# Performance work log

Measured on AMD Instinct MI355X. Metric: run time of the kernel, lower is better.

## Reference

```python
import jax, jax.numpy as jnp
import numpy as np

# Static graph structure: gene nodes first, GO-term nodes last (mask is sorted).
N_GENE, N_GOID = 40000, 10000
N = N_GENE + N_GOID
E = 800000
INPUT_DIM, H1, H2, OUT_DIM, GOID_DIM = 1280, 256, 128, 64, 4096


def setup_inputs() -> dict:
    key = jax.random.key(0)
    ks = jax.random.split(key, 16)
    s = 0.02
    return {
        "x": jax.random.normal(ks[0], (N, GOID_DIM), jnp.float32),
        "edge_index": jax.random.randint(ks[1], (2, E), 0, N),
        "mask": jnp.concatenate([jnp.ones(N_GENE, bool), jnp.zeros(N_GOID, bool)]),
        # goid_dnn: Linear(4096,1024) -> ReLU -> Linear(1024,INPUT_DIM) -> ReLU
        "Wd1": jax.random.normal(ks[2], (GOID_DIM, 1024), jnp.float32) * s,
        "bd1": jnp.zeros((1024,), jnp.float32),
        "Wd2": jax.random.normal(ks[3], (1024, INPUT_DIM), jnp.float32) * s,
        "bd2": jnp.zeros((INPUT_DIM,), jnp.float32),
        # GCNConv layers
        "W1": jax.random.normal(ks[4], (INPUT_DIM, H1), jnp.float32) * s,
        "b1": jnp.zeros((H1,), jnp.float32),
        "W2": jax.random.normal(ks[5], (H1, H2), jnp.float32) * s,
        "b2": jnp.zeros((H2,), jnp.float32),
        # goid projections
        "Wp1": jax.random.normal(ks[6], (INPUT_DIM, H1), jnp.float32) * s,
        "bp1": jnp.zeros((H1,), jnp.float32),
        "Wp2": jax.random.normal(ks[7], (H1, H2), jnp.float32) * s,
        "bp2": jnp.zeros((H2,), jnp.float32),
        # final fc
        "Wf": jax.random.normal(ks[8], (H2, OUT_DIM), jnp.float32) * s,
        "bf": jnp.zeros((OUT_DIM,), jnp.float32),
    }


def gcn_conv(x, W, b, src, dst):
    """PyG GCNConv: xW, then sym-normalized (A + I) aggregation, then bias."""
    # degree over targets with self-loops already appended to (src, dst)
    deg = jax.ops.segment_sum(jnp.ones_like(dst, x.dtype), dst, num_segments=N)
    dinv = jnp.where(deg > 0, jax.lax.rsqrt(deg), 0.0)
    norm = dinv[src] * dinv[dst]                       # [E+N]
    xw = x @ W                                          # [N, F_out]
    msg = xw[src] * norm[:, None]                       # gather-scale, [E+N, F_out]
    return jax.ops.segment_sum(msg, dst, num_segments=N) + b


def reference(x, edge_index, mask, Wd1, bd1, Wd2, bd2, W1, b1, W2, b2,
              Wp1, bp1, Wp2, bp2, Wf, bf):
    del mask  # structurally: first N_GENE rows are genes, rest are GO terms
    loop = jnp.arange(N, dtype=edge_index.dtype)
    src = jnp.concatenate([edge_index[0], loop])
    dst = jnp.concatenate([edge_index[1], loop])

    gene_x = x[:N_GENE, :INPUT_DIM]
    goid_x = x[N_GENE:]
    # goid_dnn runs under torch.no_grad() -> stop_gradient
    goid_t = jax.lax.stop_gradient(
        jax.nn.relu(jax.nn.relu(goid_x @ Wd1 + bd1) @ Wd2 + bd2))

    x_t = jnp.concatenate([gene_x, goid_t], axis=0)      # [N, INPUT_DIM]
    h1 = jax.nn.relu(gcn_conv(x_t, W1, b1, src, dst))    # dropout disabled (eval)
    p1 = goid_t @ Wp1 + bp1                              # goid_proj1
    h1 = h1.at[N_GENE:].set(p1)                          # masked scatter assign
    h2 = jax.nn.relu(gcn_conv(h1, W2, b2, src, dst))
    h2 = h2.at[N_GENE:].set(p1 @ Wp2 + bp2)              # goid_proj2(goid_proj1(...))
    return h2 @ Wf + bf                                  # [N, OUT_DIM]
```

## Files before the change

kernel.cpp:

```cpp
#include <hip/hip_runtime.h>

constexpr int kNGene = 40000;
constexpr int kNGoid = 10000;
constexpr int kN     = 50000;
constexpr int kE     = 800000;
constexpr int kInDim = 1280;
constexpr int kH1    = 256;
constexpr int kH2    = 128;
constexpr int kOut   = 64;
constexpr int kGDim  = 4096;
constexpr int kD1    = 1024;

typedef short bf16x8 __attribute__((ext_vector_type(8)));
typedef float f32x4  __attribute__((ext_vector_type(4)));

static __device__ __forceinline__ short f2bf(float f) {
  union { float f; unsigned u; } v; v.f = f;
  unsigned r = v.u + 0x7FFF + ((v.u >> 16) & 1);
  return (short)(r >> 16);
}
static __device__ __forceinline__ float bf2f(short s) {
  union { unsigned u; float f; } v;
  v.u = ((unsigned)(unsigned short)s) << 16;
  return v.f;
}
static __device__ __forceinline__ void gld16(const void* g, void* l) {
  __builtin_amdgcn_global_load_lds(
      (const __attribute__((address_space(1))) void*)g,
      (__attribute__((address_space(3))) void*)l, 16, 0, 0);
}

__global__ __launch_bounds__(256)
void k_cvt_rows(const float* __restrict__ src, int lda, short* __restrict__ dst,
                int rows, int cols) {
  int chunks_per_row = cols >> 3;
  long long total = (long long)rows * chunks_per_row;
  long long stride = (long long)gridDim.x * blockDim.x;
  for (long long i = blockIdx.x * (long long)blockDim.x + threadIdx.x; i < total; i += stride) {
    int r = (int)(i / chunks_per_row);
    int c = (int)(i - (long long)r * chunks_per_row) << 3;
    const float* sp = src + (size_t)r * lda + c;
    float4 v0 = *reinterpret_cast<const float4*>(sp);
    float4 v1 = *reinterpret_cast<const float4*>(sp + 4);
    bf16x8 t;
    t[0]=f2bf(v0.x); t[1]=f2bf(v0.y); t[2]=f2bf(v0.z); t[3]=f2bf(v0.w);
    t[4]=f2bf(v1.x); t[5]=f2bf(v1.y); t[6]=f2bf(v1.z); t[7]=f2bf(v1.w);
    *reinterpret_cast<bf16x8*>(dst + (size_t)r * cols + c) = t;
  }
}

__global__ void k_init(float* deg, int* gcount) {
  int i = blockIdx.x * blockDim.x + threadIdx.x;
  if (i < kN) deg[i] = 1.0f;
  if (i == 0) *gcount = 0;
}
__global__ void k_deg_hist(const int* __restrict__ ei, float* __restrict__ deg) {
  int e = blockIdx.x * blockDim.x + threadIdx.x;
  if (e < kE) atomicAdd(&deg[ei[kE + e]], 1.0f);
}
__global__ void k_rowassign(const float* __restrict__ deg, int* __restrict__ rowstart,
                            int* __restrict__ cursor, int* __restrict__ gcount) {
  int i = blockIdx.x * blockDim.x + threadIdx.x;
  int lane = threadIdx.x & 63;
  int c = (i < kNGene) ? ((int)deg[i] - 1) : 0;
  int incl = c;
#pragma unroll
  for (int off = 1; off < 64; off <<= 1) {
    int t = __shfl_up(incl, off, 64);
    if (lane >= off) incl += t;
  }
  int total = __shfl(incl, 63, 64);
  int base = 0;
  if (lane == 63) base = atomicAdd(gcount, total);
  base = __shfl(base, 63, 64);
  if (i < kNGene) {
    int s = base + incl - c;
    rowstart[i] = s;
    cursor[i] = s;
  }
}
__global__ void k_fill(const int* __restrict__ ei, const float* __restrict__ deg,
                       int* __restrict__ cursor, int2* __restrict__ edges) {
  int e = blockIdx.x * blockDim.x + threadIdx.x;
  if (e >= kE) return;
  int dst = ei[kE + e];
  if (dst >= kNGene) return;
  int src = ei[e];
  int pos = atomicAdd(&cursor[dst], 1);
  float nrm = rsqrtf(deg[src] * deg[dst]);
  edges[pos] = make_int2(src, __float_as_int(nrm));
}

template <int F, int OBF>
__global__ __launch_bounds__(256)
void k_gather_bf(const short* __restrict__ xw, const float* __restrict__ deg,
                 const int* __restrict__ rowstart, const int2* __restrict__ edges,
                 const float* __restrict__ bias, void* __restrict__ hv) {
  constexpr int VEC = F / 64;
  int row = (blockIdx.x * blockDim.x + threadIdx.x) >> 6;
  int lane = threadIdx.x & 63;
  if (row >= kNGene) return;
  float dg = deg[row];
  float inv = 1.0f / dg;
  float acc[VEC];
  {
    const short* xr = xw + (size_t)row * F + lane * VEC;
    if constexpr (VEC == 4) {
      short4 s = *reinterpret_cast<const short4*>(xr);
      acc[0] = bf2f(s.x) * inv; acc[1] = bf2f(s.y) * inv;
      acc[2] = bf2f(s.z) * inv; acc[3] = bf2f(s.w) * inv;
    } else {
      short2 s = *reinterpret_cast<const short2*>(xr);
      acc[0] = bf2f(s.x) * inv; acc[1] = bf2f(s.y) * inv;
    }
  }
  const int2* ep = edges + rowstart[row];
  int n = (int)dg - 1;
  int e = 0;
  for (; e + 1 < n; e += 2) {
    int2 p0 = ep[e], p1 = ep[e + 1];
    float n0 = __int_as_float(p0.y), n1 = __int_as_float(p1.y);
    const short* x0 = xw + (size_t)p0.x * F + lane * VEC;
    const short* x1 = xw + (size_t)p1.x * F + lane * VEC;
    if constexpr (VEC == 4) {
      short4 s0 = *reinterpret_cast<const short4*>(x0);
      short4 s1 = *reinterpret_cast<const short4*>(x1);
      acc[0] += bf2f(s0.x) * n0; acc[1] += bf2f(s0.y) * n0;
      acc[2] += bf2f(s0.z) * n0; acc[3] += bf2f(s0.w) * n0;
      acc[0] += bf2f(s1.x) * n1; acc[1] += bf2f(s1.y) * n1;
      acc[2] += bf2f(s1.z) * n1; acc[3] += bf2f(s1.w) * n1;
    } else {
      short2 s0 = *reinterpret_cast<const short2*>(x0);
      short2 s1 = *reinterpret_cast<const short2*>(x1);
      acc[0] += bf2f(s0.x) * n0; acc[1] += bf2f(s0.y) * n0;
      acc[0] += bf2f(s1.x) * n1; acc[1] += bf2f(s1.y) * n1;
    }
  }
  if (e < n) {
    int2 p0 = ep[e];
    float n0 = __int_as_float(p0.y);
    const short* x0 = xw + (size_t)p0.x * F + lane * VEC;
    if constexpr (VEC == 4) {
      short4 s0 = *reinterpret_cast<const short4*>(x0);
      acc[0] += bf2f(s0.x) * n0; acc[1] += bf2f(s0.y) * n0;
      acc[2] += bf2f(s0.z) * n0; acc[3] += bf2f(s0.w) * n0;
    } else {
      short2 s0 = *reinterpret_cast<const short2*>(x0);
      acc[0] += bf2f(s0.x) * n0; acc[1] += bf2f(s0.y) * n0;
    }
  }
#pragma unroll
  for (int v = 0; v < VEC; ++v) acc[v] = fmaxf(acc[v] + bias[lane * VEC + v], 0.f);
  if constexpr (OBF) {
    short* hp = (short*)hv + (size_t)row * F + lane * VEC;
    if constexpr (VEC == 4) {
      short4 o; o.x = f2bf(acc[0]); o.y = f2bf(acc[1]); o.z = f2bf(acc[2]); o.w = f2bf(acc[3]);
      *reinterpret_cast<short4*>(hp) = o;
    } else {
      short2 o; o.x = f2bf(acc[0]); o.y = f2bf(acc[1]);
      *reinterpret_cast<short2*>(hp) = o;
    }
  } else {
    float* hp = (float*)hv + (size_t)row * F + lane * VEC;
    if constexpr (VEC == 4) {
      float4 o; o.x = acc[0]; o.y = acc[1]; o.z = acc[2]; o.w = acc[3];
      *reinterpret_cast<float4*>(hp) = o;
    } else {
      float2 o; o.x = acc[0]; o.y = acc[1];
      *reinterpret_cast<float2*>(hp) = o;
    }
  }
}

__global__ __launch_bounds__(256)
void k_wtrans(const float* __restrict__ W, short* __restrict__ Wt, int K, int N) {
  __shared__ float t[32][33];
  int tx = threadIdx.x & 31, ty = threadIdx.x >> 5;
  int n0 = blockIdx.x * 32, k0 = blockIdx.y * 32;
#pragma unroll
  for (int p = 0; p < 4; ++p)
    t[ty + 8 * p][tx] = W[(size_t)(k0 + ty + 8 * p) * N + n0 + tx];
  __syncthreads();
#pragma unroll
  for (int p = 0; p < 4; ++p)
    Wt[(size_t)(n0 + ty + 8 * p) * K + k0 + tx] = f2bf(t[tx][ty + 8 * p]);
}

template <int RELU, int OBF>
__global__ __launch_bounds__(256)
void k_gemm_bf16a(const short* __restrict__ A, int lda,
                  const short* __restrict__ Bt,
                  const float* __restrict__ bias,
                  void* __restrict__ Cv, int ldc,
                  short* __restrict__ C2,
                  int M, int K)
{
  __shared__ __align__(16) short As[2][128 * 32];
  __shared__ __align__(16) short Bs[2][128 * 32];
  const int tid  = threadIdx.x;
  const int lane = tid & 63;
  const int wid  = tid >> 6;
  const int wr = wid >> 1, wc = wid & 1;
  const int row0 = blockIdx.y * 128;
  const int col0 = blockIdx.x * 128;
  const int l15 = lane & 15, l4 = lane >> 4;
  const int srow = lane >> 2, schunk = lane & 3;

  f32x4 acc[4][4] = {};

  auto stage = [&](int buf, int k0) {
#pragma unroll
    for (int q = 0; q < 2; ++q) {
      int seg = wid * 2 + q;
      int r = seg * 16 + srow;
      int grow = row0 + r;
      if (grow >= M) grow = M - 1;
      gld16(A + (size_t)grow * lda + k0 + schunk * 8, &As[buf][seg * 512]);
      int gcol = col0 + r;
      gld16(Bt + (size_t)gcol * K + k0 + schunk * 8, &Bs[buf][seg * 512]);
    }
  };

  stage(0, 0);
  __syncthreads();
  int cur = 0;
  for (int k0 = 0; k0 < K; k0 += 32) {
    if (k0 + 32 < K) stage(cur ^ 1, k0 + 32);
    bf16x8 af[4], bfr[4];
#pragma unroll
    for (int m = 0; m < 4; ++m)
      af[m] = *reinterpret_cast<bf16x8*>(&As[cur][(wr * 64 + m * 16 + l15) * 32 + l4 * 8]);
#pragma unroll
    for (int n = 0; n < 4; ++n)
      bfr[n] = *reinterpret_cast<bf16x8*>(&Bs[cur][(wc * 64 + n * 16 + l15) * 32 + l4 * 8]);
#pragma unroll
    for (int m = 0; m < 4; ++m)
#pragma unroll
      for (int n = 0; n < 4; ++n)
        acc[m][n] = __builtin_amdgcn_mfma_f32_16x16x32_bf16(af[m], bfr[n], acc[m][n], 0, 0, 0);
    __syncthreads();
    cur ^= 1;
  }

#pragma unroll
  for (int n = 0; n < 4; ++n) {
    int col = col0 + wc * 64 + n * 16 + l15;
    float bv = bias ? bias[col] : 0.f;
#pragma unroll
    for (int m = 0; m < 4; ++m) {
      int rb = row0 + wr * 64 + m * 16 + l4 * 4;
#pragma unroll
      for (int e = 0; e < 4; ++e) {
        int r = rb + e;
        if (r < M) {
          float v = acc[m][n][e] + bv;
          if (RELU) v = fmaxf(v, 0.f);
          size_t idx = (size_t)r * ldc + col;
          if constexpr (OBF) ((short*)Cv)[idx] = f2bf(v);
          else {
            ((float*)Cv)[idx] = v;
            if (C2) C2[idx] = f2bf(v);
          }
        }
      }
    }
  }
}

__global__ __launch_bounds__(256)
void k_gemm_combo(const short* __restrict__ A, int lda,
                  const short* __restrict__ Bt,
                  const float* __restrict__ bp1,
                  short* __restrict__ X1, float* __restrict__ P1,
                  short* __restrict__ H1, int M, int K)
{
  __shared__ __align__(16) short As[2][128 * 32];
  __shared__ __align__(16) short Bs[2][128 * 32];
  const int tid  = threadIdx.x;
  const int lane = tid & 63;
  const int wid  = tid >> 6;
  const int wr = wid >> 1, wc = wid & 1;
  const int row0 = blockIdx.y * 128;
  const int col0 = blockIdx.x * 128;
  const int l15 = lane & 15, l4 = lane >> 4;
  const int srow = lane >> 2, schunk = lane & 3;

  f32x4 acc[4][4] = {};

  auto stage = [&](int buf, int k0) {
#pragma unroll
    for (int q = 0; q < 2; ++q) {
      int seg = wid * 2 + q;
      int r = seg * 16 + srow;
      int grow = row0 + r;
      if (grow >= M) grow = M - 1;
      gld16(A + (size_t)grow * lda + k0 + schunk * 8, &As[buf][seg * 512]);
      int gcol = col0 + r;
      gld16(Bt + (size_t)gcol * K + k0 + schunk * 8, &Bs[buf][seg * 512]);
    }
  };

  stage(0, 0);
  __syncthreads();
  int cur = 0;
  for (int k0 = 0; k0 < K; k0 += 32) {
    if (k0 + 32 < K) stage(cur ^ 1, k0 + 32);
    bf16x8 af[4], bfr[4];
#pragma unroll
    for (int m = 0; m < 4; ++m)
      af[m] = *reinterpret_cast<bf16x8*>(&As[cur][(wr * 64 + m * 16 + l15) * 32 + l4 * 8]);
#pragma unroll
    for (int n = 0; n < 4; ++n)
      bfr[n] = *reinterpret_cast<bf16x8*>(&Bs[cur][(wc * 64 + n * 16 + l15) * 32 + l4 * 8]);
#pragma unroll
    for (int m = 0; m < 4; ++m)
#pragma unroll
      for (int n = 0; n < 4; ++n)
        acc[m][n] = __builtin_amdgcn_mfma_f32_16x16x32_bf16(af[m], bfr[n], acc[m][n], 0, 0, 0);
    __syncthreads();
    cur ^= 1;
  }

  const int is_p1 = (col0 >= 256);
#pragma unroll
  for (int n = 0; n < 4; ++n) {
    int col = col0 + wc * 64 + n * 16 + l15;
    int cl = col - (is_p1 ? 256 : 0);
    float bv = is_p1 ? bp1[cl] : 0.f;
#pragma unroll
    for (int m = 0; m < 4; ++m) {
      int rb = row0 + wr * 64 + m * 16 + l4 * 4;
#pragma unroll
      for (int e = 0; e < 4; ++e) {
        int r = rb + e;
        if (r < M) {
          float v = acc[m][n][e] + bv;
          size_t idx = (size_t)r * 256 + cl;
          if (is_p1) { P1[idx] = v; H1[idx] = f2bf(v); }
          else       { X1[idx] = f2bf(v); }
        }
      }
    }
  }
}

__global__ __launch_bounds__(512)
void k_gemm_gene(const float* __restrict__ A, int lda,
                 const short* __restrict__ Bt,
                 short* __restrict__ C,
                 int M, int K)
{
  __shared__ short As[128 * 40];
  __shared__ __align__(16) short Bs[256 * 32];
  const int tid  = threadIdx.x;
  const int lane = tid & 63;
  const int wid  = tid >> 6;
  const int wr = wid >> 2;
  const int wc = wid & 3;
  const int row0 = blockIdx.x * 128;
  const int l15 = lane & 15, l4 = lane >> 4;

  f32x4 acc[4][4] = {};
  const int sr = tid >> 2;
  const int sc = tid & 3;
  const int srow = lane >> 2, schunk = lane & 3;

  for (int k0 = 0; k0 < K; k0 += 32) {
#pragma unroll
    for (int q = 0; q < 2; ++q) {
      int seg = wid * 2 + q;
      int gcol = seg * 16 + srow;
      gld16(Bt + (size_t)gcol * K + k0 + schunk * 8, &Bs[seg * 512]);
    }
    {
      int grow = row0 + sr;
      float4 v0 = make_float4(0.f,0.f,0.f,0.f), v1 = v0;
      if (grow < M) {
        const float* ap = A + (size_t)grow * lda + k0 + sc * 8;
        v0 = *reinterpret_cast<const float4*>(ap);
        v1 = *reinterpret_cast<const float4*>(ap + 4);
      }
      bf16x8 t;
      t[0]=f2bf(v0.x); t[1]=f2bf(v0.y); t[2]=f2bf(v0.z); t[3]=f2bf(v0.w);
      t[4]=f2bf(v1.x); t[5]=f2bf(v1.y); t[6]=f2bf(v1.z); t[7]=f2bf(v1.w);
      *reinterpret_cast<bf16x8*>(&As[sr * 40 + sc * 8]) = t;
    }
    __syncthreads();

    bf16x8 af[4], bfr[4];
#pragma unroll
    for (int m = 0; m < 4; ++m)
      af[m] = *reinterpret_cast<bf16x8*>(&As[(wr * 64 + m * 16 + l15) * 40 + l4 * 8]);
#pragma unroll
    for (int n = 0; n < 4; ++n)
      bfr[n] = *reinterpret_cast<bf16x8*>(&Bs[(wc * 64 + n * 16 + l15) * 32 + l4 * 8]);
#pragma unroll
    for (int m = 0; m < 4; ++m)
#pragma unroll
      for (int n = 0; n < 4; ++n)
        acc[m][n] = __builtin_amdgcn_mfma_f32_16x16x32_bf16(af[m], bfr[n], acc[m][n], 0, 0, 0);
    __syncthreads();
  }

#pragma unroll
  for (int n = 0; n < 4; ++n) {
    int col = wc * 64 + n * 16 + l15;
#pragma unroll
    for (int m = 0; m < 4; ++m) {
      int rb = row0 + wr * 64 + m * 16 + l4 * 4;
#pragma unroll
      for (int e = 0; e < 4; ++e) {
        int r = rb + e;
        if (r < M) C[(size_t)r * 256 + col] = f2bf(acc[m][n][e]);
      }
    }
  }
}

__global__ __launch_bounds__(256)
void k_gemm_f32(const float* __restrict__ A, int lda,
                const float* __restrict__ B, int ldb,
                const float* __restrict__ bias,
                float* __restrict__ C, int ldc,
                int M, int Ncol, int K, int do_relu)
{
  __shared__ float As[16][65];
  __shared__ float Bs[16][68];
  const int tid = threadIdx.x;
  const int tx = tid & 15, ty = tid >> 4;
  const int row0 = blockIdx.y * 64;
  const int col0 = blockIdx.x * 64;
  float acc[4][4] = {};
  for (int k0 = 0; k0 < K; k0 += 16) {
    {
      int r = tid >> 2;
      int c = (tid & 3) << 2;
      int grow = row0 + r;
      float4 v = make_float4(0.f, 0.f, 0.f, 0.f);
      if (grow < M)
        v = *reinterpret_cast<const float4*>(A + (size_t)grow * lda + k0 + c);
      As[c + 0][r] = v.x; As[c + 1][r] = v.y; As[c + 2][r] = v.z; As[c + 3][r] = v.w;
    }
    {
      int r = tid >> 4;
      int c = (tid & 15) << 2;
      int gcol = col0 + c;
      float4 v = make_float4(0.f, 0.f, 0.f, 0.f);
      if (gcol < Ncol)
        v = *reinterpret_cast<const float4*>(B + (size_t)(k0 + r) * ldb + gcol);
      *reinterpret_cast<float4*>(&Bs[r][c]) = v;
    }
    __syncthreads();
#pragma unroll
    for (int k = 0; k < 16; ++k) {
      float a[4], b[4];
#pragma unroll
      for (int i = 0; i < 4; ++i) a[i] = As[k][ty + 16 * i];
#pragma unroll
      for (int j = 0; j < 4; ++j) b[j] = Bs[k][tx + 16 * j];
#pragma unroll
      for (int i = 0; i < 4; ++i)
#pragma unroll
        for (int j = 0; j < 4; ++j)
          acc[i][j] = fmaf(a[i], b[j], acc[i][j]);
    }
    __syncthreads();
  }
#pragma unroll
  for (int i = 0; i < 4; ++i) {
    int r = row0 + ty + 16 * i;
    if (r >= M) continue;
#pragma unroll
    for (int j = 0; j < 4; ++j) {
      int ccol = col0 + tx + 16 * j;
      if (ccol >= Ncol) continue;
      float v = acc[i][j];
      if (bias) v += bias[ccol];
      if (do_relu) v = fmaxf(v, 0.f);
      C[(size_t)r * ldc + ccol] = v;
    }
  }
}

extern "C" void kernel_launch(void* const* d_in, const int* in_sizes, int n_in,
                              void* d_out, int out_size, void* d_ws, size_t ws_size,
                              hipStream_t stream) {
  const float* x   = (const float*)d_in[0];
  const int*   ei  = (const int*)d_in[1];
  const float* Wd1 = (const float*)d_in[3];
  const float* bd1 = (const float*)d_in[4];
  const float* Wd2 = (const float*)d_in[5];
  const float* bd2 = (const float*)d_in[6];
  const float* W1  = (const float*)d_in[7];
  const float* b1  = (const float*)d_in[8];
  const float* W2  = (const float*)d_in[9];
  const float* b2  = (const float*)d_in[10];
  const float* Wp1 = (const float*)d_in[11];
  const float* bp1 = (const float*)d_in[12];
  const float* Wp2 = (const float*)d_in[13];
  const float* bp2 = (const float*)d_in[14];
  const float* Wf  = (const float*)d_in[15];
  const float* bf_ = (const float*)d_in[16];
  float* out = (float*)d_out;
  float* ws  = (float*)d_ws;

  short* goidx_bf = (short*)(ws + 0);
  short* goidt_bf = (short*)(ws + 20480000);
  short* h1tmp_bf = (short*)(ws + 26880000);
  short* Wd1t = (short*)(ws + 32000000);
  short* Wd2t = (short*)(ws + 34097152);
  short* W1t  = (short*)(ws + 34752512);
  short* Wp1t = (short*)(ws + 34916352);
  short* W2t  = (short*)(ws + 35080192);
  short* xw1_bf = (short*)(ws + 35100000);
  short* h1bf   = (short*)(ws + 41500000);
  float* p1     = ws + 47900000;
  short* xw2_bf = (short*)(ws + 50460000);
  float* h2     = ws + 53660000;
  float* deg    = ws + 60060000;
  int*   rowstart = (int*)(ws + 60150016);
  int*   cursor   = (int*)(ws + 60190016);
  int2*  edges    = (int2*)(ws + 60230016);
  int*   gcount   = (int*)(ws + 61830016);

  const float* gene_x = x;
  const float* goid_x = x + (size_t)kNGene * kGDim;

  auto gb = [](int M, int Ncol) { return dim3((unsigned)(Ncol / 128), (unsigned)((M + 127) / 128)); };
  auto gf = [](int M, int Ncol) { return dim3((unsigned)((Ncol + 63) / 64), (unsigned)((M + 63) / 64)); };

  k_cvt_rows<<<2048, 256, 0, stream>>>(goid_x, kGDim, goidx_bf, kNGoid, kGDim);
  k_wtrans<<<dim3(kD1 / 32, kGDim / 32), 256, 0, stream>>>(Wd1, Wd1t, kGDim, kD1);
  k_wtrans<<<dim3(kInDim / 32, kD1 / 32), 256, 0, stream>>>(Wd2, Wd2t, kD1, kInDim);
  k_wtrans<<<dim3(kH1 / 32, kInDim / 32), 256, 0, stream>>>(W1, W1t, kInDim, kH1);
  k_wtrans<<<dim3(kH1 / 32, kInDim / 32), 256, 0, stream>>>(Wp1, Wp1t, kInDim, kH1);
  k_wtrans<<<dim3(kH2 / 32, kH1 / 32), 256, 0, stream>>>(W2, W2t, kH1, kH2);

  k_init<<<(kN + 255) / 256, 256, 0, stream>>>(deg, gcount);
  k_deg_hist<<<(kE + 255) / 256, 256, 0, stream>>>(ei, deg);
  k_rowassign<<<(kNGene + 255) / 256, 256, 0, stream>>>(deg, rowstart, cursor, gcount);
  k_fill<<<(kE + 255) / 256, 256, 0, stream>>>(ei, deg, cursor, edges);

  k_gemm_bf16a<1,1><<<gb(kNGoid, kD1), 256, 0, stream>>>(goidx_bf, kGDim, Wd1t, bd1,
                                                         h1tmp_bf, kD1, nullptr, kNGoid, kGDim);
  k_gemm_bf16a<1,1><<<gb(kNGoid, kInDim), 256, 0, stream>>>(h1tmp_bf, kD1, Wd2t, bd2,
                                                            goidt_bf, kInDim, nullptr, kNGoid, kD1);

  k_gemm_gene<<<dim3((kNGene + 127) / 128), 512, 0, stream>>>(gene_x, kGDim, W1t,
                                                              xw1_bf, kNGene, kInDim);

  k_gemm_combo<<<dim3(4, (kNGoid + 127) / 128), 256, 0, stream>>>(
      goidt_bf, kInDim, W1t , bp1,
      xw1_bf + (size_t)kNGene * kH1, p1, h1bf + (size_t)kNGene * kH1,
      kNGoid, kInDim);

  k_gather_bf<kH1,1><<<(kNGene * 64 + 255) / 256, 256, 0, stream>>>(
      xw1_bf, deg, rowstart, edges, b1, h1bf);

  k_gemm_bf16a<0,1><<<gb(kN, kH2), 256, 0, stream>>>(h1bf, kH1, W2t, nullptr,
                                                     xw2_bf, kH2, nullptr, kN, kH1);

  k_gather_bf<kH2,0><<<(kNGene * 64 + 255) / 256, 256, 0, stream>>>(
      xw2_bf, deg, rowstart, edges, b2, h2);
  k_gemm_f32<<<gf(kNGoid, kH2), 256, 0, stream>>>(p1, kH1, Wp2, kH2, bp2,
                                                  h2 + (size_t)kNGene * kH2, kH2,
                                                  kNGoid, kH2, kH1, 0);

  k_gemm_f32<<<gf(kN, kOut), 256, 0, stream>>>(h2, kH2, Wf, kOut, bf_, out, kOut,
                                               kN, kOut, kH2, 0);
}
```

Measured before the change: 684.1 us.

## Widen GEMM tiles, double-buffer gene GEMM, merge weight transposes, bf16 proj2

The five weight-transpose launches become one kernel that also transposes Wp2. The goid DNN GEMMs and the combo GEMM move to 128x256 tiles with 512 threads, and the DNN GEMMs get an XCD-aware block swizzle. The gene GEMM gains double-buffered LDS staging so loads overlap MFMA. The fp32 P1 buffer is dropped, and proj2 now runs as a bf16 MFMA GEMM on the bf16 copy of p1, which adds rounding error in exchange for less memory traffic and fewer launches.

```diff
diff --git a/kernel.cpp b/kernel.cpp
--- a/kernel.cpp
+++ b/kernel.cpp
@@ -173,10 +173,24 @@
 }
 
 __global__ __launch_bounds__(256)
-void k_wtrans(const float* __restrict__ W, short* __restrict__ Wt, int K, int N) {
+void k_wtrans_all(const float* __restrict__ Wd1, short* __restrict__ Wd1t,
+                  const float* __restrict__ Wd2, short* __restrict__ Wd2t,
+                  const float* __restrict__ W1,  short* __restrict__ W1t,
+                  const float* __restrict__ Wp1, short* __restrict__ Wp1t,
+                  const float* __restrict__ W2,  short* __restrict__ W2t,
+                  const float* __restrict__ Wp2, short* __restrict__ Wp2t) {
   __shared__ float t[32][33];
+  int b = blockIdx.x;
+  const float* W; short* Wt; int K, N, bi;
+  if (b < 4096)      { W = Wd1; Wt = Wd1t; K = 4096; N = 1024; bi = b; }
+  else if (b < 5376) { W = Wd2; Wt = Wd2t; K = 1024; N = 1280; bi = b - 4096; }
+  else if (b < 5696) { W = W1;  Wt = W1t;  K = 1280; N = 256;  bi = b - 5376; }
+  else if (b < 6016) { W = Wp1; Wt = Wp1t; K = 1280; N = 256;  bi = b - 5696; }
+  else if (b < 6048) { W = W2;  Wt = W2t;  K = 256;  N = 128;  bi = b - 6016; }
+  else               { W = Wp2; Wt = Wp2t; K = 256;  N = 128;  bi = b - 6048; }
+  int nbx = N >> 5;
+  int n0 = (bi % nbx) * 32, k0 = (bi / nbx) * 32;
   int tx = threadIdx.x & 31, ty = threadIdx.x >> 5;
-  int n0 = blockIdx.x * 32, k0 = blockIdx.y * 32;
 #pragma unroll
   for (int p = 0; p < 4; ++p)
     t[ty + 8 * p][tx] = W[(size_t)(k0 + ty + 8 * p) * N + n0 + tx];
@@ -192,7 +206,6 @@
                   const short* __restrict__ Bt,
                   const float* __restrict__ bias,
                   void* __restrict__ Cv, int ldc,
-                  short* __restrict__ C2,
                   int M, int K)
 {
   __shared__ __align__(16) short As[2][128 * 32];
@@ -257,31 +270,33 @@
           if (RELU) v = fmaxf(v, 0.f);
           size_t idx = (size_t)r * ldc + col;
           if constexpr (OBF) ((short*)Cv)[idx] = f2bf(v);
-          else {
-            ((float*)Cv)[idx] = v;
-            if (C2) C2[idx] = f2bf(v);
-          }
+          else               ((float*)Cv)[idx] = v;
         }
       }
     }
   }
 }
 
-__global__ __launch_bounds__(256)
-void k_gemm_combo(const short* __restrict__ A, int lda,
-                  const short* __restrict__ Bt,
-                  const float* __restrict__ bp1,
-                  short* __restrict__ X1, float* __restrict__ P1,
-                  short* __restrict__ H1, int M, int K)
+template <int RELU, int OBF>
+__global__ __launch_bounds__(512)
+void k_gemm_wide(const short* __restrict__ A, int lda,
+                 const short* __restrict__ Bt,
+                 const float* __restrict__ bias,
+                 void* __restrict__ Cv, int ldc,
+                 int M, int K)
 {
   __shared__ __align__(16) short As[2][128 * 32];
-  __shared__ __align__(16) short Bs[2][128 * 32];
+  __shared__ __align__(16) short Bs[2][256 * 32];
   const int tid  = threadIdx.x;
   const int lane = tid & 63;
   const int wid  = tid >> 6;
-  const int wr = wid >> 1, wc = wid & 1;
-  const int row0 = blockIdx.y * 128;
-  const int col0 = blockIdx.x * 128;
+  const int wr = wid >> 2, wc = wid & 3;
+  int nwg = gridDim.x * gridDim.y;
+  int b0 = blockIdx.y * gridDim.x + blockIdx.x;
+  int qq = nwg >> 3, rr = nwg & 7, xcd = b0 & 7, j = b0 >> 3;
+  int swz = ((xcd < rr) ? xcd * (qq + 1) : rr * (qq + 1) + (xcd - rr) * qq) + j;
+  const int row0 = (swz / gridDim.x) * 128;
+  const int col0 = (swz % gridDim.x) * 256;
   const int l15 = lane & 15, l4 = lane >> 4;
   const int srow = lane >> 2, schunk = lane & 3;
 
@@ -289,14 +304,16 @@
 
   auto stage = [&](int buf, int k0) {
 #pragma unroll
-    for (int q = 0; q < 2; ++q) {
-      int seg = wid * 2 + q;
-      int r = seg * 16 + srow;
-      int grow = row0 + r;
-      if (grow >= M) grow = M - 1;
-      gld16(A + (size_t)grow * lda + k0 + schunk * 8, &As[buf][seg * 512]);
-      int gcol = col0 + r;
-      gld16(Bt + (size_t)gcol * K + k0 + schunk * 8, &Bs[buf][seg * 512]);
+    for (int q = 0; q < 3; ++q) {
+      int s = wid * 3 + q;
+      if (s < 8) {
+        int grow = row0 + s * 16 + srow;
+        if (grow >= M) grow = M - 1;
+        gld16(A + (size_t)grow * lda + k0 + schunk * 8, &As[buf][s * 512]);
+      } else {
+        int gcol = col0 + (s - 8) * 16 + srow;
+        gld16(Bt + (size_t)gcol * K + k0 + schunk * 8, &Bs[buf][(s - 8) * 512]);
+      }
     }
   };
 
@@ -321,12 +338,10 @@
     cur ^= 1;
   }
 
-  const int is_p1 = (col0 >= 256);
 #pragma unroll
   for (int n = 0; n < 4; ++n) {
     int col = col0 + wc * 64 + n * 16 + l15;
-    int cl = col - (is_p1 ? 256 : 0);
-    float bv = is_p1 ? bp1[cl] : 0.f;
+    float bv = bias ? bias[col] : 0.f;
 #pragma unroll
     for (int m = 0; m < 4; ++m) {
       int rb = row0 + wr * 64 + m * 16 + l4 * 4;
@@ -335,10 +350,85 @@
         int r = rb + e;
         if (r < M) {
           float v = acc[m][n][e] + bv;
-          size_t idx = (size_t)r * 256 + cl;
-          if (is_p1) { P1[idx] = v; H1[idx] = f2bf(v); }
-          else       { X1[idx] = f2bf(v); }
+          if (RELU) v = fmaxf(v, 0.f);
+          size_t idx = (size_t)r * ldc + col;
+          if constexpr (OBF) ((short*)Cv)[idx] = f2bf(v);
+          else               ((float*)Cv)[idx] = v;
         }
+      }
+    }
+  }
+}
+
+__global__ __launch_bounds__(512)
+void k_combo_wide(const short* __restrict__ A, int lda,
+                  const short* __restrict__ Bt,
+                  const float* __restrict__ bp1,
+                  short* __restrict__ X1, short* __restrict__ H1,
+                  int M, int K)
+{
+  __shared__ __align__(16) short As[2][128 * 32];
+  __shared__ __align__(16) short Bs[2][256 * 32];
+  const int tid  = threadIdx.x;
+  const int lane = tid & 63;
+  const int wid  = tid >> 6;
+  const int wr = wid >> 2, wc = wid & 3;
+  const int row0 = blockIdx.y * 128;
+  const int col0 = blockIdx.x * 256;
+  const int l15 = lane & 15, l4 = lane >> 4;
+  const int srow = lane >> 2, schunk = lane & 3;
+
+  f32x4 acc[4][4] = {};
+
+  auto stage = [&](int buf, int k0) {
+#pragma unroll
+    for (int q = 0; q < 3; ++q) {
+      int s = wid * 3 + q;
+      if (s < 8) {
+        int grow = row0 + s * 16 + srow;
+        if (grow >= M) grow = M - 1;
+        gld16(A + (size_t)grow * lda + k0 + schunk * 8, &As[buf][s * 512]);
+      } else {
+        int gcol = col0 + (s - 8) * 16 + srow;
+        gld16(Bt + (size_t)gcol * K + k0 + schunk * 8, &Bs[buf][(s - 8) * 512]);
+      }
+    }
+  };
+
+  stage(0, 0);
+  __syncthreads();
+  int cur = 0;
+  for (int k0 = 0; k0 < K; k0 += 32) {
+    if (k0 + 32 < K) stage(cur ^ 1, k0 + 32);
+    bf16x8 af[4], bfr[4];
+#pragma unroll
+    for (int m = 0; m < 4; ++m)
+      af[m] = *reinterpret_cast<bf16x8*>(&As[cur][(wr * 64 + m * 16 + l15) * 32 + l4 * 8]);
+#pragma unroll
+    for (int n = 0; n < 4; ++n)
+      bfr[n] = *reinterpret_cast<bf16x8*>(&Bs[cur][(wc * 64 + n * 16 + l15) * 32 + l4 * 8]);
+#pragma unroll
+    for (int m = 0; m < 4; ++m)
+#pragma unroll
+      for (int n = 0; n < 4; ++n)
+        acc[m][n] = __builtin_amdgcn_mfma_f32_16x16x32_bf16(af[m], bfr[n], acc[m][n], 0, 0, 0);
+    __syncthreads();
+    cur ^= 1;
+  }
+
+  const int is_p1 = (col0 >= 256);
+  short* dstp = is_p1 ? H1 : X1;
+#pragma unroll
+  for (int n = 0; n < 4; ++n) {
+    int cl = wc * 64 + n * 16 + l15;
+    float bv = is_p1 ? bp1[cl] : 0.f;
+#pragma unroll
+    for (int m = 0; m < 4; ++m) {
+      int rb = row0 + wr * 64 + m * 16 + l4 * 4;
+#pragma unroll
+      for (int e = 0; e < 4; ++e) {
+        int r = rb + e;
+        if (r < M) dstp[(size_t)r * 256 + cl] = f2bf(acc[m][n][e] + bv);
       }
     }
   }
@@ -350,56 +440,60 @@
                  short* __restrict__ C,
                  int M, int K)
 {
-  __shared__ short As[128 * 40];
-  __shared__ __align__(16) short Bs[256 * 32];
+  __shared__ short As[2][128 * 40];
+  __shared__ __align__(16) short Bs[2][256 * 32];
   const int tid  = threadIdx.x;
   const int lane = tid & 63;
   const int wid  = tid >> 6;
-  const int wr = wid >> 2;
-  const int wc = wid & 3;
+  const int wr = wid >> 2, wc = wid & 3;
   const int row0 = blockIdx.x * 128;
   const int l15 = lane & 15, l4 = lane >> 4;
+  const int sr = tid >> 2, sc = tid & 3;
+  const int srow = lane >> 2, schunk = lane & 3;
 
   f32x4 acc[4][4] = {};
-  const int sr = tid >> 2;
-  const int sc = tid & 3;
-  const int srow = lane >> 2, schunk = lane & 3;
-
-  for (int k0 = 0; k0 < K; k0 += 32) {
+
+  auto stageB = [&](int buf, int k0) {
 #pragma unroll
     for (int q = 0; q < 2; ++q) {
       int seg = wid * 2 + q;
       int gcol = seg * 16 + srow;
-      gld16(Bt + (size_t)gcol * K + k0 + schunk * 8, &Bs[seg * 512]);
-    }
-    {
-      int grow = row0 + sr;
-      float4 v0 = make_float4(0.f,0.f,0.f,0.f), v1 = v0;
-      if (grow < M) {
-        const float* ap = A + (size_t)grow * lda + k0 + sc * 8;
-        v0 = *reinterpret_cast<const float4*>(ap);
-        v1 = *reinterpret_cast<const float4*>(ap + 4);
-      }
-      bf16x8 t;
-      t[0]=f2bf(v0.x); t[1]=f2bf(v0.y); t[2]=f2bf(v0.z); t[3]=f2bf(v0.w);
-      t[4]=f2bf(v1.x); t[5]=f2bf(v1.y); t[6]=f2bf(v1.z); t[7]=f2bf(v1.w);
-      *reinterpret_cast<bf16x8*>(&As[sr * 40 + sc * 8]) = t;
-    }
-    __syncthreads();
-
+      gld16(Bt + (size_t)gcol * K + k0 + schunk * 8, &Bs[buf][seg * 512]);
+    }
+  };
+  auto stageA = [&](int buf, int k0) {
+    int grow = row0 + sr;
+    float4 v0 = make_float4(0.f,0.f,0.f,0.f), v1 = v0;
+    if (grow < M) {
+      const float* ap = A + (size_t)grow * lda + k0 + sc * 8;
+      v0 = *reinterpret_cast<const float4*>(ap);
+      v1 = *reinterpret_cast<const float4*>(ap + 4);
+    }
+    bf16x8 t;
+    t[0]=f2bf(v0.x); t[1]=f2bf(v0.y); t[2]=f2bf(v0.z); t[3]=f2bf(v0.w);
+    t[4]=f2bf(v1.x); t[5]=f2bf(v1.y); t[6]=f2bf(v1.z); t[7]=f2bf(v1.w);
+    *reinterpret_cast<bf16x8*>(&As[buf][sr * 40 + sc * 8]) = t;
+  };
+
+  stageB(0, 0); stageA(0, 0);
+  __syncthreads();
+  int cur = 0;
+  for (int k0 = 0; k0 < K; k0 += 32) {
+    if (k0 + 32 < K) { stageB(cur ^ 1, k0 + 32); stageA(cur ^ 1, k0 + 32); }
     bf16x8 af[4], bfr[4];
 #pragma unroll
     for (int m = 0; m < 4; ++m)
-      af[m] = *reinterpret_cast<bf16x8*>(&As[(wr * 64 + m * 16 + l15) * 40 + l4 * 8]);
+      af[m] = *reinterpret_cast<bf16x8*>(&As[cur][(wr * 64 + m * 16 + l15) * 40 + l4 * 8]);
 #pragma unroll
     for (int n = 0; n < 4; ++n)
-      bfr[n] = *reinterpret_cast<bf16x8*>(&Bs[(wc * 64 + n * 16 + l15) * 32 + l4 * 8]);
+      bfr[n] = *reinterpret_cast<bf16x8*>(&Bs[cur][(wc * 64 + n * 16 + l15) * 32 + l4 * 8]);
 #pragma unroll
     for (int m = 0; m < 4; ++m)
 #pragma unroll
       for (int n = 0; n < 4; ++n)
         acc[m][n] = __builtin_amdgcn_mfma_f32_16x16x32_bf16(af[m], bfr[n], acc[m][n], 0, 0, 0);
     __syncthreads();
+    cur ^= 1;
   }
 
 #pragma unroll
@@ -514,7 +608,6 @@
   short* W2t  = (short*)(ws + 35080192);
   short* xw1_bf = (short*)(ws + 35100000);
   short* h1bf   = (short*)(ws + 41500000);
-  float* p1     = ws + 47900000;
   short* xw2_bf = (short*)(ws + 50460000);
   float* h2     = ws + 53660000;
   float* deg    = ws + 60060000;
@@ -522,49 +615,48 @@
   int*   cursor   = (int*)(ws + 60190016);
   int2*  edges    = (int2*)(ws + 60230016);
   int*   gcount   = (int*)(ws + 61830016);
+  short* Wp2t = (short*)(ws + 61830032);
 
   const float* gene_x = x;
   const float* goid_x = x + (size_t)kNGene * kGDim;
 
   auto gb = [](int M, int Ncol) { return dim3((unsigned)(Ncol / 128), (unsigned)((M + 127) / 128)); };
+  auto gw = [](int M, int Ncol) { return dim3((unsigned)(Ncol / 256), (unsigned)((M + 127) / 128)); };
   auto gf = [](int M, int Ncol) { return dim3((unsigned)((Ncol + 63) / 64), (unsigned)((M + 63) / 64)); };
 
   k_cvt_rows<<<2048, 256, 0, stream>>>(goid_x, kGDim, goidx_bf, kNGoid, kGDim);
-  k_wtrans<<<dim3(kD1 / 32, kGDim / 32), 256, 0, stream>>>(Wd1, Wd1t, kGDim, kD1);
-  k_wtrans<<<dim3(kInDim / 32, kD1 / 32), 256, 0, stream>>>(Wd2, Wd2t, kD1, kInDim);
-  k_wtrans<<<dim3(kH1 / 32, kInDim / 32), 256, 0, stream>>>(W1, W1t, kInDim, kH1);
-  k_wtrans<<<dim3(kH1 / 32, kInDim / 32), 256, 0, stream>>>(Wp1, Wp1t, kInDim, kH1);
-  k_wtrans<<<dim3(kH2 / 32, kH1 / 32), 256, 0, stream>>>(W2, W2t, kH1, kH2);
+  k_wtrans_all<<<6080, 256, 0, stream>>>(Wd1, Wd1t, Wd2, Wd2t, W1, W1t,
+                                         Wp1, Wp1t, W2, W2t, Wp2, Wp2t);
 
   k_init<<<(kN + 255) / 256, 256, 0, stream>>>(deg, gcount);
   k_deg_hist<<<(kE + 255) / 256, 256, 0, stream>>>(ei, deg);
   k_rowassign<<<(kNGene + 255) / 256, 256, 0, stream>>>(deg, rowstart, cursor, gcount);
   k_fill<<<(kE + 255) / 256, 256, 0, stream>>>(ei, deg, cursor, edges);
 
-  k_gemm_bf16a<1,1><<<gb(kNGoid, kD1), 256, 0, stream>>>(goidx_bf, kGDim, Wd1t, bd1,
-                                                         h1tmp_bf, kD1, nullptr, kNGoid, kGDim);
-  k_gemm_bf16a<1,1><<<gb(kNGoid, kInDim), 256, 0, stream>>>(h1tmp_bf, kD1, Wd2t, bd2,
-                                                            goidt_bf, kInDim, nullptr, kNGoid, kD1);
+  k_gemm_wide<1,1><<<gw(kNGoid, kD1), 512, 0, stream>>>(goidx_bf, kGDim, Wd1t, bd1,
+                                                        h1tmp_bf, kD1, kNGoid, kGDim);
+  k_gemm_wide<1,1><<<gw(kNGoid, kInDim), 512, 0, stream>>>(h1tmp_bf, kD1, Wd2t, bd2,
+                                                           goidt_bf, kInDim, kNGoid, kD1);
 
   k_gemm_gene<<<dim3((kNGene + 127) / 128), 512, 0, stream>>>(gene_x, kGDim, W1t,
                                                               xw1_bf, kNGene, kInDim);
 
-  k_gemm_combo<<<dim3(4, (kNGoid + 127) / 128), 256, 0, stream>>>(
+  k_combo_wide<<<dim3(2, (kNGoid + 127) / 128), 512, 0, stream>>>(
       goidt_bf, kInDim, W1t , bp1,
-      xw1_bf + (size_t)kNGene * kH1, p1, h1bf + (size_t)kNGene * kH1,
+      xw1_bf + (size_t)kNGene * kH1, h1bf + (size_t)kNGene * kH1,
       kNGoid, kInDim);
 
   k_gather_bf<kH1,1><<<(kNGene * 64 + 255) / 256, 256, 0, stream>>>(
       xw1_bf, deg, rowstart, edges, b1, h1bf);
 
   k_gemm_bf16a<0,1><<<gb(kN, kH2), 256, 0, stream>>>(h1bf, kH1, W2t, nullptr,
-                                                     xw2_bf, kH2, nullptr, kN, kH1);
+                                                     xw2_bf, kH2, kN, kH1);
 
   k_gather_bf<kH2,0><<<(kNGene * 64 + 255) / 256, 256, 0, stream>>>(
       xw2_bf, deg, rowstart, edges, b2, h2);
-  k_gemm_f32<<<gf(kNGoid, kH2), 256, 0, stream>>>(p1, kH1, Wp2, kH2, bp2,
-                                                  h2 + (size_t)kNGene * kH2, kH2,
-                                                  kNGoid, kH2, kH1, 0);
+  k_gemm_bf16a<0,0><<<gb(kNGoid, kH2), 256, 0, stream>>>(
+      h1bf + (size_t)kNGene * kH1, kH1, Wp2t, bp2,
+      h2 + (size_t)kNGene * kH2, kH2, kNGoid, kH1);
 
   k_gemm_f32<<<gf(kN, kOut), 256, 0, stream>>>(h2, kH2, Wf, kOut, bf_, out, kOut,
                                                kN, kOut, kH2, 0);
```

New measurement: 610.6 us. 10.7% less time.
